# Performance work log

Measured on AMD Instinct MI355X. Metric: run time of the kernel, lower is better.

Reference implementation:

```python
import jax, jax.numpy as jnp
import numpy as np

N, F_IN, HID, PROJ, K = 10000, 256, 128, 64, 50
E, HEADS = 320000, 8


def _p(key, shape, scale=0.05):
    return jax.random.normal(key, shape, dtype=jnp.float32) * scale


def setup_inputs() -> dict:
    key = jax.random.key(0)
    ks = jax.random.split(key, 20)
    x = jax.random.normal(ks[0], (N, F_IN), dtype=jnp.float32)
    edge_index = jax.random.randint(ks[1], (2, E), 0, N, dtype=jnp.int64)
    return {
        "x": x,
        "edge_index": edge_index,
        "lin1_w": _p(ks[2], (HID, F_IN)), "lin1_b": _p(ks[3], (HID,)),
        "gat1_w": _p(ks[4], (HEADS * HID, F_IN)),
        "gat1_att_src": _p(ks[5], (HEADS, HID)), "gat1_att_dst": _p(ks[6], (HEADS, HID)),
        "gat1_b": _p(ks[7], (HEADS * HID,)),
        "gat2_w": _p(ks[8], (HID, HEADS * HID)),
        "gat2_att_src": _p(ks[9], (1, HID)), "gat2_att_dst": _p(ks[10], (1, HID)),
        "gat2_b": _p(ks[11], (HID,)),
        "proj_w": _p(ks[12], (PROJ, 2 * HID)), "proj_b": _p(ks[13], (PROJ,)),
        "ln_g": jnp.ones((2 * HID,), jnp.float32), "ln_b": jnp.zeros((2 * HID,), jnp.float32),
        "lin_w": _p(ks[14], (64, 4 * HID)), "lin_b": _p(ks[15], (64,)),
    }


def gat_conv(x, src, dst, W, a_src, a_dst, b, concat):
    # PyG GATConv, add_self_loops=False, eval mode (no attention dropout).
    H, C = a_src.shape
    n = x.shape[0]
    h = (x @ W.T).reshape(n, H, C)                      # [N,H,C]
    al_src = jnp.einsum('nhc,hc->nh', h, a_src)          # [N,H]
    al_dst = jnp.einsum('nhc,hc->nh', h, a_dst)
    e = jax.nn.leaky_relu(al_src[src] + al_dst[dst], 0.2)  # [E,H]
    emax = jax.ops.segment_max(e, dst, num_segments=n)
    ex = jnp.exp(e - emax[dst])
    denom = jax.ops.segment_sum(ex, dst, num_segments=n) + 1e-16
    alpha = ex / denom[dst]                              # [E,H]
    out = jax.ops.segment_sum(h[src] * alpha[:, :, None], dst, num_segments=n)  # [N,H,C]
    if concat:
        return out.reshape(n, H * C) + b
    return out.mean(axis=1) + b


def knn_mean(g_score, final, k):
    # dense pairwise sq-distance + top-k (replaces CPU KDTree loop), gather-mean
    sq = jnp.sum(g_score * g_score, axis=1)
    neg_d2 = 2.0 * (g_score @ g_score.T) - sq[:, None] - sq[None, :]
    idx = jax.lax.top_k(jax.lax.stop_gradient(neg_d2), k)[1]  # [N,k]
    return jnp.mean(final[idx], axis=1)                        # [N,2h]


def reference(x, edge_index, lin1_w, lin1_b, gat1_w, gat1_att_src, gat1_att_dst,
              gat1_b, gat2_w, gat2_att_src, gat2_att_dst, gat2_b, proj_w, proj_b,
              ln_g, ln_b, lin_w, lin_b):
    src, dst = edge_index[0], edge_index[1]
    x1 = jax.nn.relu(x @ lin1_w.T + lin1_b)                              # MLP branch
    xg = jax.nn.relu(gat_conv(x, src, dst, gat1_w, gat1_att_src, gat1_att_dst, gat1_b, True))
    x2 = gat_conv(xg, src, dst, gat2_w, gat2_att_src, gat2_att_dst, gat2_b, False)
    final = jnp.concatenate([x1, x2], axis=1)                            # [N,2h]
    g_score = final @ proj_w.T + proj_b                                  # [N,proj]
    sim = knn_mean(g_score, final, K)                                    # [N,2h]
    mu = sim.mean(axis=-1, keepdims=True)
    var = sim.var(axis=-1, keepdims=True)
    sim = (sim - mu) * jax.lax.rsqrt(var + 1e-5) * ln_g + ln_b           # LayerNorm
    out = jnp.concatenate([final, sim], axis=1) @ lin_w.T + lin_b        # [N,64]
    return out
```

## Files before the change

kernel.cpp:

```cpp
#include <hip/hip_runtime.h>

#define FIN 256
#define KNN 50
#define CAP 192
#define J1  512
#define MAXJC 3208

static __device__ __forceinline__ float lrelu02(float v){ return v > 0.f ? v : 0.2f*v; }
static __device__ __forceinline__ unsigned fkey(float v){
  unsigned u = __float_as_uint(v);
  return (u & 0x80000000u) ? ~u : (u | 0x80000000u);
}

__global__ __launch_bounds__(256) void k_zero_int(int* p, int n){
  int i = blockIdx.x*256 + threadIdx.x; if (i<n) p[i]=0;
}
__global__ __launch_bounds__(256) void k_count_deg(const int* __restrict__ dstv, int* deg, int E){
  int i = blockIdx.x*256 + threadIdx.x; if (i<E) atomicAdd(&deg[dstv[i]], 1);
}
__global__ __launch_bounds__(256) void k_scan(const int* __restrict__ deg, int* offs, int* cursor, int n){
  __shared__ int buf[256]; __shared__ int carry;
  int t = threadIdx.x;
  if (t==0) carry = 0;
  __syncthreads();
  for (int base=0; base<n; base+=256){
    int v = (base+t<n)? deg[base+t] : 0;
    buf[t]=v; __syncthreads();
    for (int off=1; off<256; off<<=1){
      int add = (t>=off)? buf[t-off] : 0;
      __syncthreads();
      buf[t]+=add; __syncthreads();
    }
    int excl = buf[t]-v+carry;
    if (base+t<n){ offs[base+t]=excl; cursor[base+t]=excl; }
    __syncthreads();
    if (t==0) carry += buf[255];
    __syncthreads();
  }
}
__global__ __launch_bounds__(256) void k_fill_csr(const int* __restrict__ dstv, int* cursor, int* csr, int E){
  int i = blockIdx.x*256 + threadIdx.x;
  if (i<E){ int p=atomicAdd(&cursor[dstv[i]],1); csr[p]=i; }
}
__global__ __launch_bounds__(64) void k_sort_csr_wave(int* csr, const int* __restrict__ offs, const int* __restrict__ deg, int n){
  int node = blockIdx.x; if (node>=n) return;
  int t = threadIdx.x;
  int st = offs[node], d = deg[node];
  __shared__ int buf[256];
  if (d > 256){
    if (t==0){
      for (int a=1;a<d;++a){ int v=csr[st+a]; int b=a-1;
        while (b>=0 && csr[st+b]>v){ csr[st+b+1]=csr[st+b]; --b; }
        csr[st+b+1]=v; }
    }
    return;
  }
  for (int q=t;q<d;q+=64) buf[q]=csr[st+q];
  __syncthreads();
  for (int it=0; it<d; ++it){
    int ph = it & 1;
    for (int pidx=t; 2*pidx+ph+1 < d; pidx+=64){
      int a = 2*pidx+ph;
      int va=buf[a], vb=buf[a+1];
      if (va > vb){ buf[a]=vb; buf[a+1]=va; }
    }
    __syncthreads();
  }
  for (int q=t;q<d;q+=64) csr[st+q]=buf[q];
}

__global__ __launch_bounds__(256) void k_fold(
  const float* __restrict__ W, const float* __restrict__ as8, const float* __restrict__ ad8,
  float* __restrict__ Wf)
{
  int o = blockIdx.x;
  int t = threadIdx.x;
  int h = o & 7;
  const float* av = (o<8) ? (as8 + h*128) : (ad8 + h*128);
  const float* wp = W + (size_t)h*128*256 + t;
  float acc = 0.f;
  #pragma unroll 4
  for (int c=0;c<128;++c) acc += av[c] * wp[(size_t)c*256];
  Wf[o*256+t] = acc;
}

__global__ __launch_bounds__(256) void gemm_bt(
    const float* __restrict__ A, int lda,
    const float* __restrict__ W, int ldw,
    const float* __restrict__ bias,
    float* __restrict__ C, int ldc, int coff,
    int M, int Kdim, int O, int relu,
    int az, int wz, int cz, int bz)
{
  A += (size_t)blockIdx.z * az;
  W += (size_t)blockIdx.z * wz;
  if (bias) bias += (size_t)blockIdx.z * bz;
  coff += blockIdx.z * cz;
  __shared__ float As[32][68];
  __shared__ float Ws[32][68];
  int t  = threadIdx.x;
  int n0 = blockIdx.y * 64;
  int o0 = blockIdx.x * 64;
  int tx = t & 15, ty = t >> 4;
  float acc[4][4] = {};
  int kgrp = t & 7;
  int row  = t >> 3;
  for (int k0 = 0; k0 < Kdim; k0 += 32) {
    #pragma unroll
    for (int p = 0; p < 2; ++p) {
      int r = row + 32*p;
      int n = n0 + r;
      float4 v = make_float4(0.f,0.f,0.f,0.f);
      if (n < M) v = *(const float4*)(A + (size_t)n*lda + k0 + 4*kgrp);
      As[4*kgrp+0][r] = v.x; As[4*kgrp+1][r] = v.y;
      As[4*kgrp+2][r] = v.z; As[4*kgrp+3][r] = v.w;
      int o = o0 + r;
      float4 w = make_float4(0.f,0.f,0.f,0.f);
      if (o < O) w = *(const float4*)(W + (size_t)o*ldw + k0 + 4*kgrp);
      Ws[4*kgrp+0][r] = w.x; Ws[4*kgrp+1][r] = w.y;
      Ws[4*kgrp+2][r] = w.z; Ws[4*kgrp+3][r] = w.w;
    }
    __syncthreads();
    #pragma unroll 8
    for (int kk = 0; kk < 32; ++kk) {
      float4 a = *(const float4*)&As[kk][ty*4];
      float4 w = *(const float4*)&Ws[kk][tx*4];
      float av[4] = {a.x,a.y,a.z,a.w};
      float wv[4] = {w.x,w.y,w.z,w.w};
      #pragma unroll
      for (int i=0;i<4;++i)
        #pragma unroll
        for (int j=0;j<4;++j) acc[i][j] += av[i]*wv[j];
    }
    __syncthreads();
  }
  #pragma unroll
  for (int i=0;i<4;++i) {
    int n = n0 + ty*4 + i;
    if (n >= M) continue;
    #pragma unroll
    for (int j=0;j<4;++j) {
      int o = o0 + tx*4 + j;
      if (o >= O) continue;
      float v = acc[i][j] + (bias ? bias[o] : 0.f);
      if (relu) v = fmaxf(v, 0.f);
      C[(size_t)n*ldc + coff + o] = v;
    }
  }
}

__global__ __launch_bounds__(256) void gemm128(
    const float* __restrict__ A, int lda,
    const float* __restrict__ W, int ldw,
    const float* __restrict__ bias,
    float* __restrict__ C, int ldc, int coff,
    int M, int Kdim, int relu,
    int az, int wz, int cz, int bz)
{
  A += (size_t)blockIdx.z * az;
  W += (size_t)blockIdx.z * wz;
  const float* bp = bias + (size_t)blockIdx.z * bz;
  int ccol = coff + blockIdx.z * cz;
  __shared__ float As[32][132];
  __shared__ float Ws[32][132];
  int t = threadIdx.x;
  int n0 = blockIdx.y * 128;
  int kg = t & 7, rb = t >> 3;
  int tx = t & 15, ty = t >> 4;
  float acc[2][2][4][4] = {};
  for (int k0 = 0; k0 < Kdim; k0 += 32) {
    __syncthreads();
    #pragma unroll
    for (int p = 0; p < 4; ++p) {
      int r = rb + 32*p;
      int n = n0 + r;
      float4 v = make_float4(0.f,0.f,0.f,0.f);
      if (n < M) v = *(const float4*)(A + (size_t)n*lda + k0 + 4*kg);
      As[4*kg+0][r]=v.x; As[4*kg+1][r]=v.y; As[4*kg+2][r]=v.z; As[4*kg+3][r]=v.w;
      float4 w = *(const float4*)(W + (size_t)r*ldw + k0 + 4*kg);
      Ws[4*kg+0][r]=w.x; Ws[4*kg+1][r]=w.y; Ws[4*kg+2][r]=w.z; Ws[4*kg+3][r]=w.w;
    }
    __syncthreads();
    #pragma unroll 8
    for (int kk = 0; kk < 32; ++kk) {
      float4 A0 = *(const float4*)&As[kk][ty*4];
      float4 A1 = *(const float4*)&As[kk][64+ty*4];
      float4 B0 = *(const float4*)&Ws[kk][tx*4];
      float4 B1 = *(const float4*)&Ws[kk][64+tx*4];
      float av[2][4] = {{A0.x,A0.y,A0.z,A0.w},{A1.x,A1.y,A1.z,A1.w}};
      float bv[2][4] = {{B0.x,B0.y,B0.z,B0.w},{B1.x,B1.y,B1.z,B1.w}};
      #pragma unroll
      for (int pi=0;pi<2;++pi)
        #pragma unroll
        for (int pj=0;pj<2;++pj)
          #pragma unroll
          for (int i=0;i<4;++i)
            #pragma unroll
            for (int j=0;j<4;++j)
              acc[pi][pj][i][j] += av[pi][i]*bv[pj][j];
    }
  }
  #pragma unroll
  for (int pi=0;pi<2;++pi)
    #pragma unroll
    for (int i=0;i<4;++i) {
      int n = n0 + pi*64 + ty*4 + i;
      if (n >= M) continue;
      #pragma unroll
      for (int pj=0;pj<2;++pj)
        #pragma unroll
        for (int j=0;j<4;++j) {
          int o = pj*64 + tx*4 + j;
          float v = acc[pi][pj][i][j] + bp[o];
          if (relu) v = fmaxf(v, 0.f);
          C[(size_t)n*ldc + ccol + o] = v;
        }
    }
}

__global__ __launch_bounds__(256) void gemm_h2(
    const float* __restrict__ A, const float* __restrict__ W,
    float* __restrict__ C, int M)
{
  __shared__ float4 AiS[32*16];
  __shared__ float4 WjS[32*16];
  float* Aif = (float*)AiS;
  float* Wjf = (float*)WjS;
  int t = threadIdx.x;
  int o0 = blockIdx.x * 64;
  int i0 = blockIdx.y * 64;
  int tx = t & 15, ty = t >> 4;
  int kg = t & 7, rw = t >> 3;
  float acc[4][4] = {};
  for (int h=0; h<32; ++h) {
    if (h) __syncthreads();
    #pragma unroll
    for (int rr=0; rr<2; ++rr) {
      int r = rw + 32*rr;
      int slot = (r>>2) ^ kg;
      int gi = i0 + r;
      float4 v = (gi<M) ? *(const float4*)(A + (size_t)gi*1024 + h*32 + 4*kg) : make_float4(0,0,0,0);
      Aif[((4*kg+0)*16 + slot)*4 + (r&3)] = v.x;
      Aif[((4*kg+1)*16 + slot)*4 + (r&3)] = v.y;
      Aif[((4*kg+2)*16 + slot)*4 + (r&3)] = v.z;
      Aif[((4*kg+3)*16 + slot)*4 + (r&3)] = v.w;
      float4 w = *(const float4*)(W + (size_t)(o0+r)*1024 + h*32 + 4*kg);
      Wjf[((4*kg+0)*16 + slot)*4 + (r&3)] = w.x;
      Wjf[((4*kg+1)*16 + slot)*4 + (r&3)] = w.y;
      Wjf[((4*kg+2)*16 + slot)*4 + (r&3)] = w.z;
      Wjf[((4*kg+3)*16 + slot)*4 + (r&3)] = w.w;
    }
    __syncthreads();
    #pragma unroll 8
    for (int k=0; k<32; ++k) {
      int kc3 = (k>>2)&7;
      float4 A0 = AiS[k*16 + (ty ^ kc3)];
      float4 B0 = WjS[k*16 + (tx ^ kc3)];
      float av[4] = {A0.x,A0.y,A0.z,A0.w};
      float bv[4] = {B0.x,B0.y,B0.z,B0.w};
      #pragma unroll
      for (int i=0;i<4;++i)
        #pragma unroll
        for (int j=0;j<4;++j)
          acc[i][j] += av[i]*bv[j];
    }
  }
  #pragma unroll
  for (int i=0;i<4;++i){
    int n = i0 + ty*4 + i;
    if (n >= M) continue;
    float4 v4 = make_float4(acc[i][0], acc[i][1], acc[i][2], acc[i][3]);
    *(float4*)(C + (size_t)n*128 + o0 + tx*4) = v4;
  }
}

__global__ __launch_bounds__(256) void att_logits(
    const float* __restrict__ hbuf, const float* __restrict__ asrc,
    const float* __restrict__ adst, float* __restrict__ als, float* __restrict__ ald,
    int H, int M)
{
  int gidx = blockIdx.x*256 + threadIdx.x;
  if (gidx >= M*H) return;
  int n = gidx / H, h = gidx % H;
  const float* hp = hbuf + (size_t)n*H*128 + (size_t)h*128;
  const float* as = asrc + h*128;
  const float* ad = adst + h*128;
  float s1=0.f, s2=0.f;
  for (int c=0;c<128;++c){ float v=hp[c]; s1 += v*as[c]; s2 += v*ad[c]; }
  als[gidx]=s1; ald[gidx]=s2;
}

template<int NH>
__global__ __launch_bounds__(256) void gat1_agg_x(
    const float* __restrict__ x, const float* __restrict__ al1,
    const int* __restrict__ csr, const int* __restrict__ offs, const int* __restrict__ deg,
    const int* __restrict__ srcv,
    float* __restrict__ agg, int h0, int M)
{
  const int n = blockIdx.x, t = threadIdx.x;
  const int d = deg[n], st = offs[n];
  const int lane = t & 63, w = t >> 6;
  __shared__ float sh_ald[NH];
  __shared__ float wpart[4*NH];
  __shared__ float emax_s[NH], den_s[NH];
  __shared__ int   s_lds[128];
  __shared__ float alpha_lds[128*NH];
  if (t < NH) sh_ald[t] = al1[(size_t)n*16 + 8 + h0 + t];
  __syncthreads();
  float lm[NH];
  #pragma unroll
  for (int h=0;h<NH;++h) lm[h] = -__builtin_inff();
  for (int q=t; q<d; q+=256) {
    int s = srcv[csr[st+q]];
    float av[NH];
    float4 a0 = *(const float4*)(al1 + (size_t)s*16 + h0);
    av[0]=a0.x; av[1]=a0.y; av[2]=a0.z; av[3]=a0.w;
    if constexpr (NH==8){
      float4 a1 = *(const float4*)(al1 + (size_t)s*16 + h0 + 4);
      av[4]=a1.x; av[5]=a1.y; av[6]=a1.z; av[7]=a1.w;
    }
    #pragma unroll
    for (int h=0;h<NH;++h) lm[h] = fmaxf(lm[h], lrelu02(av[h] + sh_ald[h]));
  }
  #pragma unroll
  for (int h=0;h<NH;++h){
    float v = lm[h];
    for (int off=32;off>0;off>>=1) v = fmaxf(v, __shfl_down(v, off, 64));
    if (lane==0) wpart[w*NH+h] = v;
  }
  __syncthreads();
  if (t < NH)
    emax_s[t] = fmaxf(fmaxf(wpart[t], wpart[NH+t]), fmaxf(wpart[2*NH+t], wpart[3*NH+t]));
  __syncthreads();
  float ls[NH];
  #pragma unroll
  for (int h=0;h<NH;++h) ls[h]=0.f;
  for (int q=t; q<d; q+=256) {
    int s = srcv[csr[st+q]];
    float av[NH];
    float4 a0 = *(const float4*)(al1 + (size_t)s*16 + h0);
    av[0]=a0.x; av[1]=a0.y; av[2]=a0.z; av[3]=a0.w;
    if constexpr (NH==8){
      float4 a1 = *(const float4*)(al1 + (size_t)s*16 + h0 + 4);
      av[4]=a1.x; av[5]=a1.y; av[6]=a1.z; av[7]=a1.w;
    }
    #pragma unroll
    for (int h=0;h<NH;++h) ls[h] += expf(lrelu02(av[h] + sh_ald[h]) - emax_s[h]);
  }
  #pragma unroll
  for (int h=0;h<NH;++h){
    float v = ls[h];
    for (int off=32;off>0;off>>=1) v += __shfl_down(v, off, 64);
    if (lane==0) wpart[w*NH+h] = v;
  }
  __syncthreads();
  if (t < NH)
    den_s[t] = wpart[t] + wpart[NH+t] + wpart[2*NH+t] + wpart[3*NH+t] + 1e-16f;
  float acc[NH];
  #pragma unroll
  for (int h=0;h<NH;++h) acc[h]=0.f;
  for (int c0=0; c0<d; c0+=128) {
    int cl = min(128, d-c0);
    __syncthreads();
    for (int q=t; q<cl; q+=256) s_lds[q] = srcv[csr[st+c0+q]];
    __syncthreads();
    for (int idx=t; idx<cl*NH; idx+=256) {
      int q = idx / NH, h = idx % NH;
      float als = al1[(size_t)s_lds[q]*16 + h0 + h];
      float v = lrelu02(als + sh_ald[h]);
      alpha_lds[q*NH+h] = expf(v - emax_s[h]) / den_s[h];
    }
    __syncthreads();
    for (int q=0; q<cl; ++q) {
      float xv = x[(size_t)s_lds[q]*FIN + t];
      #pragma unroll
      for (int h=0;h<NH;++h) acc[h] += alpha_lds[q*NH+h] * xv;
    }
  }
  #pragma unroll
  for (int h=0;h<NH;++h) agg[(size_t)n*(NH*256) + h*256 + t] = acc[h];
}

__global__ __launch_bounds__(256) void gat2_agg_wave(
  const float* __restrict__ h2, const float* __restrict__ als, const float* __restrict__ ald,
  const int* __restrict__ csr, const int* __restrict__ offs, const int* __restrict__ deg,
  const int* __restrict__ srcv, const float* __restrict__ bias,
  float* __restrict__ cat, int M)
{
  int wid = blockIdx.x*4 + (threadIdx.x>>6);
  int lane = threadIdx.x & 63;
  if (wid >= M) return;
  int d = deg[wid], st = offs[wid];
  float aldn = ald[wid];
  float lm = -__builtin_inff();
  for (int q=lane;q<d;q+=64){ int s=srcv[csr[st+q]]; lm = fmaxf(lm, lrelu02(als[s]+aldn)); }
  #pragma unroll
  for (int m=1;m<64;m<<=1) lm = fmaxf(lm, __shfl_xor(lm, m, 64));
  float ls = 0.f;
  for (int q=lane;q<d;q+=64){ int s=srcv[csr[st+q]]; ls += expf(lrelu02(als[s]+aldn)-lm); }
  #pragma unroll
  for (int m=1;m<64;m<<=1) ls += __shfl_xor(ls, m, 64);
  float den = ls + 1e-16f;
  float a0=0.f, a1=0.f;
  for (int q=0;q<d;++q){
    int s = srcv[csr[st+q]];
    float alpha = expf(lrelu02(als[s]+aldn)-lm)/den;
    float2 hv = *(const float2*)(h2 + (size_t)s*128 + lane*2);
    a0 += alpha*hv.x; a1 += alpha*hv.y;
  }
  a0 += bias[lane*2]; a1 += bias[lane*2+1];
  *(float2*)(cat + (size_t)wid*512 + 128 + lane*2) = make_float2(a0,a1);
}

__global__ __launch_bounds__(256) void k_sq(const float* __restrict__ g, float* sq, int n){
  int i = blockIdx.x*256+threadIdx.x;
  if (i<n){ const float* p=g+(size_t)i*64; float s=0.f; for(int c=0;c<64;++c) s+=p[c]*p[c]; sq[i]=s; }
}
__global__ __launch_bounds__(256) void k_init_topk(unsigned int* tk, int* ti, int n){
  int i = blockIdx.x*256+threadIdx.x;
  if (i<n){ tk[i]=0u; ti[i]=0x7fffffff; }
}

template<int MODE, int JC>
__global__ __launch_bounds__(256) void gram_k(
    const float* __restrict__ G, const float* __restrict__ sqv,
    const unsigned* __restrict__ kth,
    float* __restrict__ slab, int* __restrict__ cnt,
    unsigned* __restrict__ ck, int* __restrict__ ci,
    int j0, int M)
{
  __shared__ float4 GiS[32*16];
  __shared__ float4 GjS[32*32];
  float* Gif = (float*)GiS;
  float* Gjf = (float*)GjS;
  int t = threadIdx.x;
  int i0  = blockIdx.y * 64;
  int jt0 = blockIdx.x * 128;
  int tx = t & 15, ty = t >> 4;
  int kg = t & 7, rw = t >> 3;
  float acc[2][4][4] = {};
  #pragma unroll
  for (int h=0; h<2; ++h) {
    if (h) __syncthreads();
    #pragma unroll
    for (int rr=0; rr<2; ++rr) {
      int r = rw + 32*rr;
      int slotA = (r>>2) ^ kg;
      int gi = i0 + r;
      float4 v = (gi<M) ? *(const float4*)(G + (size_t)gi*64 + h*32 + 4*kg) : make_float4(0,0,0,0);
      Gif[((4*kg+0)*16 + slotA)*4 + (r&3)] = v.x;
      Gif[((4*kg+1)*16 + slotA)*4 + (r&3)] = v.y;
      Gif[((4*kg+2)*16 + slotA)*4 + (r&3)] = v.z;
      Gif[((4*kg+3)*16 + slotA)*4 + (r&3)] = v.w;
    }
    #pragma unroll
    for (int rr=0; rr<4; ++rr) {
      int r = rw + 32*rr;
      int slotB = (r>>2) ^ kg;
      int gj = j0 + jt0 + r;
      float4 w = (gj<M) ? *(const float4*)(G + (size_t)gj*64 + h*32 + 4*kg) : make_float4(0,0,0,0);
      Gjf[((4*kg+0)*32 + slotB)*4 + (r&3)] = w.x;
      Gjf[((4*kg+1)*32 + slotB)*4 + (r&3)] = w.y;
      Gjf[((4*kg+2)*32 + slotB)*4 + (r&3)] = w.z;
      Gjf[((4*kg+3)*32 + slotB)*4 + (r&3)] = w.w;
    }
    __syncthreads();
    #pragma unroll 8
    for (int k=0; k<32; ++k) {
      int kc3 = (k>>2)&7;
      float4 A0 = GiS[k*16 + (ty ^ kc3)];
      float4 B0 = GjS[k*32 + (tx ^ kc3)];
      float4 B1 = GjS[k*32 + 16 + (tx ^ kc3)];
      float av[4] = {A0.x,A0.y,A0.z,A0.w};
      float bv[2][4] = {{B0.x,B0.y,B0.z,B0.w},{B1.x,B1.y,B1.z,B1.w}};
      #pragma unroll
      for (int pj=0;pj<2;++pj)
        #pragma unroll
        for (int i=0;i<4;++i)
          #pragma unroll
          for (int j=0;j<4;++j)
            acc[pj][i][j] += av[i]*bv[pj][j];
    }
  }
  #pragma unroll
  for (int i=0;i<4;++i){
    int ii = i0 + ty*4 + i;
    if (ii >= M) continue;
    float sqi = sqv[ii];
    #pragma unroll
    for (int pj=0;pj<2;++pj){
      int jl0 = jt0 + pj*64 + tx*4;
      if (jl0 >= JC) continue;
      float4 v4;
      v4.x = 2.f*acc[pj][i][0] - sqi - sqv[j0+jl0+0];
      v4.y = 2.f*acc[pj][i][1] - sqi - sqv[j0+jl0+1];
      v4.z = 2.f*acc[pj][i][2] - sqi - sqv[j0+jl0+2];
      v4.w = 2.f*acc[pj][i][3] - sqi - sqv[j0+jl0+3];
      if (MODE == 0) {
        *(float4*)(slab + (size_t)ii*J1 + jl0) = v4;
      } else {
        unsigned kt = kth[ii];
        float vv[4] = {v4.x, v4.y, v4.z, v4.w};
        #pragma unroll
        for (int j=0;j<4;++j){
          unsigned key = fkey(vv[j]);
          if (key > kt){
            int pos = atomicAdd(&cnt[ii], 1);
            if (pos < CAP){ ck[(size_t)ii*CAP+pos] = key; ci[(size_t)ii*CAP+pos] = j0+jl0+j; }
          }
        }
      }
    }
  }
}

__global__ __launch_bounds__(256) void topk_radix(
    const float* __restrict__ slab, int j0, int jcount,
    unsigned* __restrict__ tkk, int* __restrict__ tki, unsigned* __restrict__ kth, int M)
{
  __shared__ unsigned keys[J1 + KNN];
  __shared__ int hist[4*256];
  __shared__ int red2[256];
  __shared__ int oldidx[KNN];
  __shared__ int outidx[KNN];
  __shared__ unsigned outkey[KNN];
  __shared__ int b_star, cnt2;
  int i = blockIdx.x, t = threadIdx.x, w = t >> 6;
  for (int p=t; p<jcount; p+=256) keys[p] = fkey(slab[(size_t)i*J1 + p]);
  if (t < KNN){ keys[jcount+t] = tkk[(size_t)i*KNN+t]; oldidx[t] = tki[(size_t)i*KNN+t]; }
  if (t == 0) cnt2 = 0;
  __syncthreads();
  const int total = jcount + KNN;
  unsigned prefix = 0, pmask = 0;
  int need = KNN;
  #pragma unroll
  for (int pass=0; pass<4; ++pass) {
    int shift = 24 - 8*pass;
    hist[t]=0; hist[256+t]=0; hist[512+t]=0; hist[768+t]=0;
    __syncthreads();
    for (int p=t; p<total; p+=256) {
      unsigned k = keys[p];
      if ((k & pmask) == prefix) atomicAdd(&hist[(w<<8) + ((k>>shift)&255)], 1);
    }
    __syncthreads();
    red2[t] = hist[t] + hist[256+t] + hist[512+t] + hist[768+t];
    __syncthreads();
    for (int off=1; off<256; off<<=1) {
      int v = (t+off<256) ? red2[t+off] : 0;
      __syncthreads();
      red2[t] += v;
      __syncthreads();
    }
    if (red2[t] >= need && (t==255 || red2[t+1] < need)) b_star = t;
    __syncthreads();
    int b = b_star;
    need -= (b < 255) ? red2[b+1] : 0;
    prefix |= ((unsigned)b) << shift;
    pmask  |= 0xFFu << shift;
    __syncthreads();
  }
  for (int p=t; p<total; p+=256) {
    unsigned k = keys[p];
    if (k > prefix) {
      int pos = atomicAdd(&cnt2, 1);
      outidx[pos] = (p < jcount) ? (j0 + p) : oldidx[p-jcount];
      outkey[pos] = k;
    }
  }
  __syncthreads();
  int base = cnt2;
  int last = -1;
  for (int it=0; it<need; ++it) {
    int best = 0x7fffffff;
    for (int p=t; p<total; p+=256) {
      if (keys[p] == prefix) {
        int idx = (p < jcount) ? (j0 + p) : oldidx[p-jcount];
        if (idx > last && idx < best) best = idx;
      }
    }
    red2[t] = best; __syncthreads();
    for (int s=128;s>0;s>>=1){ if (t<s) red2[t] = min(red2[t], red2[t+s]); __syncthreads(); }
    if (t==0) { outidx[base+it] = red2[0]; outkey[base+it] = prefix; }
    last = red2[0];
    __syncthreads();
  }
  if (t < KNN){ tkk[(size_t)i*KNN+t] = outkey[t]; tki[(size_t)i*KNN+t] = outidx[t]; }
  if (t == 0) kth[i] = prefix;
}

__global__ __launch_bounds__(256) void topk_fast(
    const float* __restrict__ G, const float* __restrict__ sqv,
    int j0, int jcount,
    const unsigned* __restrict__ ck, const int* __restrict__ ci, const int* __restrict__ cnt,
    unsigned* __restrict__ tkk, int* __restrict__ tki, unsigned* __restrict__ kth, int M)
{
  int i = blockIdx.x, t = threadIdx.x;
  int c = cnt[i];
  if (c <= CAP) {
    __shared__ unsigned skey[256];
    __shared__ int sidx[256];
    unsigned k = 0u; int id = 0x7fffffff;
    if (t < KNN){ k = tkk[(size_t)i*KNN+t]; id = tki[(size_t)i*KNN+t]; }
    else if (t-KNN < c){ k = ck[(size_t)i*CAP + (t-KNN)]; id = ci[(size_t)i*CAP + (t-KNN)]; }
    skey[t] = k; sidx[t] = id;
    for (int size=2; size<=256; size<<=1){
      for (int stride=size>>1; stride>0; stride>>=1){
        __syncthreads();
        int p = t ^ stride;
        if (p > t){
          unsigned k1=skey[t], k2=skey[p]; int i1=sidx[t], i2=sidx[p];
          bool b21 = (k2>k1) || (k2==k1 && i2<i1);
          bool b12 = (k1>k2) || (k1==k2 && i1<i2);
          bool desc = ((t & size) == 0);
          if (desc ? b21 : b12){
            skey[t]=k2; skey[p]=k1; sidx[t]=i2; sidx[p]=i1;
          }
        }
      }
    }
    __syncthreads();
    if (t < KNN){ tkk[(size_t)i*KNN+t] = skey[t]; tki[(size_t)i*KNN+t] = sidx[t]; }
    if (t == 0) kth[i] = skey[KNN-1];
  } else {
    __shared__ float gvec[64];
    __shared__ unsigned keys[MAXJC + KNN];
    __shared__ int hist[256];
    __shared__ int red2[256];
    __shared__ int oldidx[KNN];
    __shared__ int outidx[KNN];
    __shared__ unsigned outkey[KNN];
    __shared__ int b_star, cnt2;
    if (t < 64) gvec[t] = G[(size_t)i*64 + t];
    if (t == 0) cnt2 = 0;
    __syncthreads();
    float sqi = sqv[i];
    for (int p=t; p<jcount; p+=256){
      const float4* gj4 = (const float4*)(G + (size_t)(j0+p)*64);
      float acc = 0.f;
      #pragma unroll 4
      for (int q=0;q<16;++q){
        float4 w = gj4[q];
        acc += gvec[4*q+0]*w.x;
        acc += gvec[4*q+1]*w.y;
        acc += gvec[4*q+2]*w.z;
        acc += gvec[4*q+3]*w.w;
      }
      keys[p] = fkey(2.f*acc - sqi - sqv[j0+p]);
    }
    if (t < KNN){ keys[jcount+t] = tkk[(size_t)i*KNN+t]; oldidx[t] = tki[(size_t)i*KNN+t]; }
    __syncthreads();
    const int total = jcount + KNN;
    unsigned prefix = 0, pmask = 0;
    int need = KNN;
    #pragma unroll
    for (int pass=0; pass<4; ++pass) {
      int shift = 24 - 8*pass;
      hist[t] = 0; __syncthreads();
      for (int p=t; p<total; p+=256) {
        unsigned k = keys[p];
        if ((k & pmask) == prefix) atomicAdd(&hist[(k>>shift)&255], 1);
      }
      __syncthreads();
      for (int off=1; off<256; off<<=1) {
        int v = (t+off<256) ? hist[t+off] : 0;
        __syncthreads();
        hist[t] += v;
        __syncthreads();
      }
      if (hist[t] >= need && (t==255 || hist[t+1] < need)) b_star = t;
      __syncthreads();
      int b = b_star;
      need -= (b < 255) ? hist[b+1] : 0;
      prefix |= ((unsigned)b) << shift;
      pmask  |= 0xFFu << shift;
      __syncthreads();
    }
    for (int p=t; p<total; p+=256) {
      unsigned k = keys[p];
      if (k > prefix) {
        int pos = atomicAdd(&cnt2, 1);
        outidx[pos] = (p < jcount) ? (j0 + p) : oldidx[p-jcount];
        outkey[pos] = k;
      }
    }
    __syncthreads();
    int base = cnt2;
    int last = -1;
    for (int it=0; it<need; ++it) {
      int best = 0x7fffffff;
      for (int p=t; p<total; p+=256) {
        if (keys[p] == prefix) {
          int idx = (p < jcount) ? (j0 + p) : oldidx[p-jcount];
          if (idx > last && idx < best) best = idx;
        }
      }
      red2[t] = best; __syncthreads();
      for (int s=128;s>0;s>>=1){ if (t<s) red2[t] = min(red2[t], red2[t+s]); __syncthreads(); }
      if (t==0) { outidx[base+it] = red2[0]; outkey[base+it] = prefix; }
      last = red2[0];
      __syncthreads();
    }
    if (t < KNN){ tkk[(size_t)i*KNN+t] = outkey[t]; tki[(size_t)i*KNN+t] = outidx[t]; }
    if (t == 0) kth[i] = prefix;
  }
}

__global__ __launch_bounds__(256) void knn_mean_ln(
    float* __restrict__ cat, const int* __restrict__ topi,
    const float* __restrict__ g, const float* __restrict__ b, int M)
{
  int i = blockIdx.x; int t = threadIdx.x;
  __shared__ int idx[KNN];
  __shared__ float red[256];
  if (t<KNN) idx[t]=topi[(size_t)i*KNN+t];
  __syncthreads();
  float acc=0.f;
  for (int r=0;r<KNN;++r) acc += cat[(size_t)idx[r]*512 + t];
  float xval = acc * (1.f/KNN);
  red[t]=xval; __syncthreads();
  for (int s=128;s>0;s>>=1){ if(t<s) red[t]+=red[t+s]; __syncthreads(); }
  float mu = red[0]*(1.f/256.f); __syncthreads();
  float d = xval-mu;
  red[t]=d*d; __syncthreads();
  for (int s=128;s>0;s>>=1){ if(t<s) red[t]+=red[t+s]; __syncthreads(); }
  float var = red[0]*(1.f/256.f);
  float y = d * rsqrtf(var+1e-5f) * g[t] + b[t];
  cat[(size_t)i*512 + 256 + t] = y;
}

extern "C" void kernel_launch(void* const* d_in, const int* in_sizes, int n_in,
                              void* d_out, int out_size, void* d_ws, size_t ws_size,
                              hipStream_t stream)
{
  const float* x      = (const float*)d_in[0];
  const int*   ei     = (const int*)  d_in[1];
  const float* lin1_w = (const float*)d_in[2];
  const float* lin1_b = (const float*)d_in[3];
  const float* gat1_w = (const float*)d_in[4];
  const float* g1_as  = (const float*)d_in[5];
  const float* g1_ad  = (const float*)d_in[6];
  const float* gat1_b = (const float*)d_in[7];
  const float* gat2_w = (const float*)d_in[8];
  const float* g2_as  = (const float*)d_in[9];
  const float* g2_ad  = (const float*)d_in[10];
  const float* gat2_b = (const float*)d_in[11];
  const float* proj_w = (const float*)d_in[12];
  const float* proj_b = (const float*)d_in[13];
  const float* ln_g   = (const float*)d_in[14];
  const float* ln_b   = (const float*)d_in[15];
  const float* lin_w  = (const float*)d_in[16];
  const float* lin_b  = (const float*)d_in[17];
  float* outp = (float*)d_out;

  const int N = in_sizes[0]/FIN;
  const int E = in_sizes[1]/2;
  const int* srcv = ei;
  const int* dstv = ei + E;

  size_t needFull = sizeof(float)*((size_t)N*(2048+1024+512+16+128+1+1+64+1+KNN+KNN+1+1+1+1+1+2*CAP) + E + 4096);
  bool full = ws_size >= needFull;
  size_t aggF = full ? (size_t)N*2048 : (size_t)N*1024;

  float* ws = (float*)d_ws;
  size_t f = 0;
  float* agg  = ws + f; f += aggF;
  float* xg   = ws + f; f += (size_t)N*1024;
  float* slab = agg;
  float* cat  = ws + f; f += (size_t)N*512;
  float* al1  = ws + f; f += (size_t)N*16;
  float* h2   = ws + f; f += (size_t)N*128;
  float* al2s = ws + f; f += (size_t)N;
  float* al2d = ws + f; f += (size_t)N;
  float* gsc  = ws + f; f += (size_t)N*64;
  float* sqv  = ws + f; f += (size_t)N;
  unsigned* tkk = (unsigned*)(ws + f); f += (size_t)N*KNN;
  int* tki    = (int*)(ws + f); f += (size_t)N*KNN;
  int* deg    = (int*)(ws + f); f += (size_t)N;
  int* offs   = (int*)(ws + f); f += (size_t)N;
  int* cursor = (int*)(ws + f); f += (size_t)N;
  unsigned* kth = (unsigned*)(ws + f); f += (size_t)N;
  int* ccnt   = (int*)(ws + f); f += (size_t)N;
  unsigned* ck = (unsigned*)(ws + f); f += (size_t)N*CAP;
  int* ci     = (int*)(ws + f); f += (size_t)N*CAP;
  int* csr    = (int*)(ws + f); f += (size_t)E;
  float* Wf   = ws + f; f += 4096;
  (void)n_in; (void)out_size;

  dim3 b256(256);
  int gy = (N+63)/64;
  int gy128 = (N+127)/128;
  int gy64 = (N+63)/64;

  k_zero_int<<<(N+255)/256, b256, 0, stream>>>(deg, N);
  k_count_deg<<<(E+255)/256, b256, 0, stream>>>(dstv, deg, E);
  k_scan<<<1, b256, 0, stream>>>(deg, offs, cursor, N);
  k_fill_csr<<<(E+255)/256, b256, 0, stream>>>(dstv, cursor, csr, E);
  k_sort_csr_wave<<<N, dim3(64), 0, stream>>>(csr, offs, deg, N);

  k_fold<<<16, b256, 0, stream>>>(gat1_w, g1_as, g1_ad, Wf);
  gemm_bt<<<dim3(1,gy,1), b256, 0, stream>>>(x,FIN, Wf,FIN, nullptr, al1,16,0, N,FIN,16, 0, 0,0,0,0);

  gemm_bt<<<dim3(2,gy,1), b256, 0, stream>>>(x,FIN, lin1_w,FIN, lin1_b, cat,512,0, N,FIN,128, 1, 0,0,0,0);

  if (full) {
    gat1_agg_x<8><<<N, b256, 0, stream>>>(x, al1, csr, offs, deg, srcv, agg, 0, N);
    gemm128<<<dim3(1,gy128,8), b256, 0, stream>>>(agg,2048, gat1_w,FIN, gat1_b, xg,1024,0,
                                                  N,FIN, 1, 256, 128*256, 128, 128);
  } else {
    for (int h0=0; h0<8; h0+=4) {
      gat1_agg_x<4><<<N, b256, 0, stream>>>(x, al1, csr, offs, deg, srcv, agg, h0, N);
      gemm128<<<dim3(1,gy128,4), b256, 0, stream>>>(agg,1024, gat1_w + (size_t)h0*128*256,FIN,
                                                    gat1_b + h0*128, xg,1024, h0*128,
                                                    N,FIN, 1, 256, 128*256, 128, 128);
    }
  }

  gemm_h2<<<dim3(2, gy64), b256, 0, stream>>>(xg, gat2_w, h2, N);
  att_logits<<<(N+255)/256, b256, 0, stream>>>(h2, g2_as, g2_ad, al2s, al2d, 1, N);
  gat2_agg_wave<<<(N+3)/4, b256, 0, stream>>>(h2, al2s, al2d, csr, offs, deg, srcv, gat2_b, cat, N);

  gemm_bt<<<dim3(1,gy,1), b256, 0, stream>>>(cat,512, proj_w,256, proj_b, gsc,64,0, N,256,64, 0, 0,0,0,0);
  k_sq<<<(N+255)/256, b256, 0, stream>>>(gsc, sqv, N);
  k_init_topk<<<(N*KNN+255)/256, b256, 0, stream>>>(tkk, tki, N*KNN);
  k_zero_int<<<(N+255)/256, b256, 0, stream>>>((int*)kth, N);

  const int sj0[5] = {0, 512, 1536, 3584, 6792};
  const int sjc[5] = {512, 1024, 2048, 3208, 3208};
  for (int s = 0; s < 5; ++s){
    int j0 = sj0[s];
    int jc = sjc[s];
    if (jc > N - j0) jc = N - j0;
    if (jc <= 0) break;
    if (s == 0) {
      gram_k<0,512><<<dim3((512+127)/128, gy64), b256, 0, stream>>>(gsc, sqv, kth, slab, ccnt, ck, ci, j0, N);
      topk_radix<<<N, b256, 0, stream>>>(slab, j0, jc, tkk, tki, kth, N);
    } else {
      k_zero_int<<<(N+255)/256, b256, 0, stream>>>(ccnt, N);
      if (s == 1)
        gram_k<1,1024><<<dim3((1024+127)/128, gy64), b256, 0, stream>>>(gsc, sqv, kth, slab, ccnt, ck, ci, j0, N);
      else if (s == 2)
        gram_k<1,2048><<<dim3((2048+127)/128, gy64), b256, 0, stream>>>(gsc, sqv, kth, slab, ccnt, ck, ci, j0, N);
      else
        gram_k<1,3208><<<dim3((3208+127)/128, gy64), b256, 0, stream>>>(gsc, sqv, kth, slab, ccnt, ck, ci, j0, N);
      topk_fast<<<N, b256, 0, stream>>>(gsc, sqv, j0, jc, ck, ci, ccnt, tkk, tki, kth, N);
    }
  }
  knn_mean_ln<<<N, b256, 0, stream>>>(cat, tki, ln_g, ln_b, N);
  gemm_bt<<<dim3(1,gy,1), b256, 0, stream>>>(cat,512, lin_w,512, lin_b, outp,64,0, N,512,64, 0, 0,0,0,0);
}
```

Baseline: 1.256 ms.

## Fuse first KNN slab gram and radix top-k; fold counter resets into top-k kernels

```diff
diff --git a/kernel.cpp b/kernel.cpp
--- a/kernel.cpp
+++ b/kernel.cpp
@@ -588,10 +588,100 @@
   if (t == 0) kth[i] = prefix;
 }
 
+__global__ __launch_bounds__(256) void topk_radix_c(
+    const float* __restrict__ G, const float* __restrict__ sqv,
+    unsigned* __restrict__ tkk, int* __restrict__ tki, unsigned* __restrict__ kth,
+    int* __restrict__ cnt, int M)
+{
+  __shared__ float gvec[64];
+  __shared__ unsigned keys[J1 + KNN];
+  __shared__ int hist[4*256];
+  __shared__ int red2[256];
+  __shared__ int outidx[KNN];
+  __shared__ unsigned outkey[KNN];
+  __shared__ int b_star, cnt2;
+  int i = blockIdx.x, t = threadIdx.x, w = t >> 6;
+  if (t < 64) gvec[t] = G[(size_t)i*64 + t];
+  if (t == 0) cnt2 = 0;
+  __syncthreads();
+  float sqi = sqv[i];
+  for (int p=t; p<J1; p+=256){
+    const float4* gj4 = (const float4*)(G + (size_t)p*64);
+    float acc = 0.f;
+    #pragma unroll 4
+    for (int q=0;q<16;++q){
+      float4 wv = gj4[q];
+      acc += gvec[4*q+0]*wv.x;
+      acc += gvec[4*q+1]*wv.y;
+      acc += gvec[4*q+2]*wv.z;
+      acc += gvec[4*q+3]*wv.w;
+    }
+    keys[p] = fkey(2.f*acc - sqi - sqv[p]);
+  }
+  if (t < KNN) keys[J1+t] = 0u;
+  __syncthreads();
+  const int total = J1 + KNN;
+  unsigned prefix = 0, pmask = 0;
+  int need = KNN;
+  #pragma unroll
+  for (int pass=0; pass<4; ++pass) {
+    int shift = 24 - 8*pass;
+    hist[t]=0; hist[256+t]=0; hist[512+t]=0; hist[768+t]=0;
+    __syncthreads();
+    for (int p=t; p<total; p+=256) {
+      unsigned k = keys[p];
+      if ((k & pmask) == prefix) atomicAdd(&hist[(w<<8) + ((k>>shift)&255)], 1);
+    }
+    __syncthreads();
+    red2[t] = hist[t] + hist[256+t] + hist[512+t] + hist[768+t];
+    __syncthreads();
+    for (int off=1; off<256; off<<=1) {
+      int v = (t+off<256) ? red2[t+off] : 0;
+      __syncthreads();
+      red2[t] += v;
+      __syncthreads();
+    }
+    if (red2[t] >= need && (t==255 || red2[t+1] < need)) b_star = t;
+    __syncthreads();
+    int b = b_star;
+    need -= (b < 255) ? red2[b+1] : 0;
+    prefix |= ((unsigned)b) << shift;
+    pmask  |= 0xFFu << shift;
+    __syncthreads();
+  }
+  for (int p=t; p<total; p+=256) {
+    unsigned k = keys[p];
+    if (k > prefix) {
+      int pos = atomicAdd(&cnt2, 1);
+      outidx[pos] = (p < J1) ? p : 0x7fffffff;
+      outkey[pos] = k;
+    }
+  }
+  __syncthreads();
+  int base = cnt2;
+  int last = -1;
+  for (int it=0; it<need; ++it) {
+    int best = 0x7fffffff;
+    for (int p=t; p<total; p+=256) {
+      if (keys[p] == prefix) {
+        int idx = (p < J1) ? p : 0x7fffffff;
+        if (idx > last && idx < best) best = idx;
+      }
+    }
+    red2[t] = best; __syncthreads();
+    for (int s=128;s>0;s>>=1){ if (t<s) red2[t] = min(red2[t], red2[t+s]); __syncthreads(); }
+    if (t==0) { outidx[base+it] = red2[0]; outkey[base+it] = prefix; }
+    last = red2[0];
+    __syncthreads();
+  }
+  if (t < KNN){ tkk[(size_t)i*KNN+t] = outkey[t]; tki[(size_t)i*KNN+t] = outidx[t]; }
+  if (t == 0){ kth[i] = prefix; cnt[i] = 0; }
+}
+
 __global__ __launch_bounds__(256) void topk_fast(
     const float* __restrict__ G, const float* __restrict__ sqv,
     int j0, int jcount,
-    const unsigned* __restrict__ ck, const int* __restrict__ ci, const int* __restrict__ cnt,
+    const unsigned* __restrict__ ck, const int* __restrict__ ci, int* __restrict__ cnt,
     unsigned* __restrict__ tkk, int* __restrict__ tki, unsigned* __restrict__ kth, int M)
 {
   int i = blockIdx.x, t = threadIdx.x;
@@ -620,7 +710,7 @@
     }
     __syncthreads();
     if (t < KNN){ tkk[(size_t)i*KNN+t] = skey[t]; tki[(size_t)i*KNN+t] = sidx[t]; }
-    if (t == 0) kth[i] = skey[KNN-1];
+    if (t == 0){ kth[i] = skey[KNN-1]; cnt[i] = 0; }
   } else {
     __shared__ float gvec[64];
     __shared__ unsigned keys[MAXJC + KNN];
@@ -701,7 +791,7 @@
       __syncthreads();
     }
     if (t < KNN){ tkk[(size_t)i*KNN+t] = outkey[t]; tki[(size_t)i*KNN+t] = outidx[t]; }
-    if (t == 0) kth[i] = prefix;
+    if (t == 0){ kth[i] = prefix; cnt[i] = 0; }
   }
 }
 
@@ -821,29 +911,28 @@
 
   gemm_bt<<<dim3(1,gy,1), b256, 0, stream>>>(cat,512, proj_w,256, proj_b, gsc,64,0, N,256,64, 0, 0,0,0,0);
   k_sq<<<(N+255)/256, b256, 0, stream>>>(gsc, sqv, N);
-  k_init_topk<<<(N*KNN+255)/256, b256, 0, stream>>>(tkk, tki, N*KNN);
-  k_zero_int<<<(N+255)/256, b256, 0, stream>>>((int*)kth, N);
-
-  const int sj0[5] = {0, 512, 1536, 3584, 6792};
-  const int sjc[5] = {512, 1024, 2048, 3208, 3208};
-  for (int s = 0; s < 5; ++s){
-    int j0 = sj0[s];
-    int jc = sjc[s];
+
+  topk_radix_c<<<N, b256, 0, stream>>>(gsc, sqv, tkk, tki, kth, ccnt, N);
+  if (N < 0) {
+    k_init_topk<<<1, b256, 0, stream>>>(tkk, tki, 0);
+    gram_k<0,512><<<dim3(4, gy64), b256, 0, stream>>>(gsc, sqv, kth, slab, ccnt, ck, ci, 0, N);
+    topk_radix<<<N, b256, 0, stream>>>(slab, 0, 512, tkk, tki, kth, N);
+  }
+
+  const int sj0f[4] = {512, 1536, 3584, 6792};
+  const int sjcf[4] = {1024, 2048, 3208, 3208};
+  for (int s = 0; s < 4; ++s){
+    int j0 = sj0f[s];
+    int jc = sjcf[s];
     if (jc > N - j0) jc = N - j0;
     if (jc <= 0) break;
-    if (s == 0) {
-      gram_k<0,512><<<dim3((512+127)/128, gy64), b256, 0, stream>>>(gsc, sqv, kth, slab, ccnt, ck, ci, j0, N);
-      topk_radix<<<N, b256, 0, stream>>>(slab, j0, jc, tkk, tki, kth, N);
-    } else {
-      k_zero_int<<<(N+255)/256, b256, 0, stream>>>(ccnt, N);
-      if (s == 1)
-        gram_k<1,1024><<<dim3((1024+127)/128, gy64), b256, 0, stream>>>(gsc, sqv, kth, slab, ccnt, ck, ci, j0, N);
-      else if (s == 2)
-        gram_k<1,2048><<<dim3((2048+127)/128, gy64), b256, 0, stream>>>(gsc, sqv, kth, slab, ccnt, ck, ci, j0, N);
-      else
-        gram_k<1,3208><<<dim3((3208+127)/128, gy64), b256, 0, stream>>>(gsc, sqv, kth, slab, ccnt, ck, ci, j0, N);
-      topk_fast<<<N, b256, 0, stream>>>(gsc, sqv, j0, jc, ck, ci, ccnt, tkk, tki, kth, N);
-    }
+    if (s == 0)
+      gram_k<1,1024><<<dim3(8, gy64), b256, 0, stream>>>(gsc, sqv, kth, slab, ccnt, ck, ci, j0, N);
+    else if (s == 1)
+      gram_k<1,2048><<<dim3(16, gy64), b256, 0, stream>>>(gsc, sqv, kth, slab, ccnt, ck, ci, j0, N);
+    else
+      gram_k<1,3208><<<dim3(26, gy64), b256, 0, stream>>>(gsc, sqv, kth, slab, ccnt, ck, ci, j0, N);
+    topk_fast<<<N, b256, 0, stream>>>(gsc, sqv, j0, jc, ck, ci, ccnt, tkk, tki, kth, N);
   }
   knn_mean_ln<<<N, b256, 0, stream>>>(cat, tki, ln_g, ln_b, N);
   gemm_bt<<<dim3(1,gy,1), b256, 0, stream>>>(cat,512, lin_w,512, lin_b, outp,64,0, N,512,64, 0, 0,0,0,0);
```

New measurement: 1.315 ms. 4.7% more time.
